# Performance work log

Hardware: AMD Instinct MI355X
Metric: run time of the kernel (lower is better)

## Reference

```python
import jax, jax.numpy as jnp
import numpy as np

M_HIST = 6
LAM = 1e-4
THRESHOLD = 50
BETA = 1.0


def _f_step(z, x, Wh, bh, Wx, bx, Wo, bo):
    # DEQ cell: f(z, x) = tanh(Linear(tanh(h_layer(x) + x_layer(z))))
    # (note: Func.forward(x, z) is called as f(z, x), so h_layer sees the
    #  external input x and x_layer sees the iterate z)
    hidden = jnp.tanh(x @ Wh.T + bh + z @ Wx.T + bx)  # [B,S,H]
    return jnp.tanh(hidden @ Wo.T + bo)               # [B,S,D]


def _anderson(f, x0):
    bsz = x0.shape[0]
    dL = x0.shape[1] * x0.shape[2]
    flat = lambda z: z.reshape(bsz, dL)
    unflat = lambda z: z.reshape(x0.shape)

    X = jnp.zeros((bsz, M_HIST, dL), dtype=x0.dtype)
    F = jnp.zeros((bsz, M_HIST, dL), dtype=x0.dtype)
    F0 = flat(f(x0))
    X = X.at[:, 0].set(flat(x0))
    F = F.at[:, 0].set(F0)
    X = X.at[:, 1].set(F0)
    F = F.at[:, 1].set(flat(f(unflat(F0))))

    lowest = jnp.asarray(1e8, dtype=x0.dtype)
    lowest_x = jnp.zeros((bsz, dL), dtype=x0.dtype)

    for k in range(2, THRESHOLD):  # fixed unrolled solver iterations
        n = min(k, M_HIST)
        G = F[:, :n] - X[:, :n]                       # [B,n,dL]
        GG = jnp.einsum('bnd,bmd->bnm', G, G) + LAM * jnp.eye(n, dtype=x0.dtype)
        H = jnp.zeros((bsz, n + 1, n + 1), dtype=x0.dtype)
        H = H.at[:, 0, 1:].set(1.0)
        H = H.at[:, 1:, 0].set(1.0)
        H = H.at[:, 1:, 1:].set(GG)
        rhs = jnp.zeros((bsz, n + 1, 1), dtype=x0.dtype).at[:, 0, 0].set(1.0)
        alpha = jnp.linalg.solve(H, rhs)[:, 1:, 0]    # [B,n]
        Xk = BETA * jnp.einsum('bn,bnd->bd', alpha, F[:, :n]) \
            + (1.0 - BETA) * jnp.einsum('bn,bnd->bd', alpha, X[:, :n])
        Fk = flat(f(unflat(Xk)))
        X = X.at[:, k % M_HIST].set(Xk)
        F = F.at[:, k % M_HIST].set(Fk)
        abs_diff = jnp.linalg.norm(Fk - Xk)
        rel_diff = abs_diff / (1e-5 + jnp.linalg.norm(Fk))
        better = rel_diff < lowest
        lowest_x = jnp.where(better, Xk, lowest_x)
        lowest = jnp.minimum(rel_diff, lowest)
    return unflat(lowest_x)


def setup_inputs() -> dict:
    key = jax.random.key(0)
    ks = jax.random.split(key, 9)
    B, S, D, H, O = 16384, 31, 14, 50, 1
    sc = lambda fan_in: 1.0 / np.sqrt(fan_in)
    return {
        'x':  jax.random.normal(ks[0], (B, S, D), jnp.float32),
        'Wh': jax.random.normal(ks[1], (H, D), jnp.float32) * sc(D),
        'bh': jax.random.normal(ks[2], (H,), jnp.float32) * sc(D),
        'Wx': jax.random.normal(ks[3], (H, D), jnp.float32) * sc(D),
        'bx': jax.random.normal(ks[4], (H,), jnp.float32) * sc(D),
        'Wo': jax.random.normal(ks[5], (D, H), jnp.float32) * sc(H),
        'bo': jax.random.normal(ks[6], (D,), jnp.float32) * sc(H),
        'Wf': jax.random.normal(ks[7], (O, S * D), jnp.float32) * sc(S * D),
        'bf': jax.random.normal(ks[8], (O,), jnp.float32) * sc(S * D),
    }


def reference(x, Wh, bh, Wx, bx, Wo, bo, Wf, bf):
    f = lambda z: _f_step(z, x, Wh, bh, Wx, bx, Wo, bo)
    z_star = _anderson(f, jnp.zeros_like(x))   # fixed-point solve (no grad)
    z = f(z_star)                              # one extra f application
    out = z.reshape(z.shape[0], -1) @ Wf.T + bf  # [B,1]
    return out
```

## Files before the change

kernel.cpp:

```cpp
#include <hip/hip_runtime.h>
#include <hip/hip_fp16.h>

#define S 31
#define D 14
#define H 50
#define MH 6
#define NB 16384
#define NITER 48
#define LAMR 1e-4f

#define WS_D2   0
#define WS_F2   64
#define WS_WHP  128
#define WS_WXP  928
#define WS_WOT  1728
#define WS_BHX  2528
#define WS_BO   2592
#define WS_OUTK 4096

#ifndef __has_builtin
#define __has_builtin(x) 0
#endif
#if __has_builtin(__builtin_amdgcn_rcpf)
#define FRCP(x) __builtin_amdgcn_rcpf(x)
#else
#define FRCP(x) (1.0f/(x))
#endif

__device__ __forceinline__ float tfast(float x){
  float e = __expf(x + x);
  return 1.f - 2.f * FRCP(e + 1.f);
}

__device__ __forceinline__ float half_red(float v){
  v += __shfl_xor(v, 1, 64);
  v += __shfl_xor(v, 2, 64);
  v += __shfl_xor(v, 4, 64);
  v += __shfl_xor(v, 8, 64);
  v += __shfl_xor(v, 16, 64);
  return v;
}

__global__ void prep_kernel(const float* __restrict__ Wh, const float* __restrict__ bh,
                            const float* __restrict__ Wx, const float* __restrict__ bx,
                            const float* __restrict__ Wo, const float* __restrict__ bo,
                            float* __restrict__ ws){
  int t = threadIdx.x;
  for (int i=t;i<128;i+=256) ws[i]=0.f;
  for (int i=t;i<800;i+=256){
    int h=i>>4, d=i&15;
    ws[WS_WHP+i] = (d<D)? Wh[h*D+d] : 0.f;
    ws[WS_WXP+i] = (d<D)? Wx[h*D+d] : 0.f;
    ws[WS_WOT+i] = (d<D)? Wo[d*H+h] : 0.f;
  }
  for (int i=t;i<64;i+=256) ws[WS_BHX+i] = (i<H)? bh[i]+bx[i] : 0.f;
  for (int i=t;i<16;i+=256) ws[WS_BO+i]  = (i<D)? bo[i] : 0.f;
}

#define FEVAL() do{ \
  float tac[D]; \
  _Pragma("unroll") for (int d_=0; d_<D; ++d_) tac[d_]=bop[d_]; \
  _Pragma("unroll 2") \
  for (int h_=0; h_<H; ++h_){ \
    const float* wxr = wxp + h_*16; \
    const float* wor = wot + h_*16; \
    float a0 = hxr[h_], a1 = 0.f; \
    _Pragma("unroll") for (int d_=0; d_<D; d_+=2){ a0 += xv[d_]*wxr[d_]; a1 += xv[d_+1]*wxr[d_+1]; } \
    float th = tfast(a0+a1); \
    _Pragma("unroll") for (int d_=0; d_<D; ++d_) tac[d_] += th*wor[d_]; \
  } \
  _Pragma("unroll") for (int d_=0; d_<D; ++d_) fv[d_] = tfast(tac[d_]); \
}while(0)

#define UPD(r) do{ \
  _Pragma("unroll") for (int dd_=0;dd_<7;++dd_){ \
    Fh[r][dd_]=__floats2half2_rn(fv[2*dd_],fv[2*dd_+1]); \
    Gh[r][dd_]=__floats2half2_rn(gv[2*dd_],gv[2*dd_+1]); } \
  _Pragma("unroll") for (int j_=0;j_<MH;++j_){ \
    float dl=0.f; \
    _Pragma("unroll") for (int dd_=0;dd_<7;++dd_){ \
      float2 g2=__half22float2(Gh[j_][dd_]); \
      dl += gv[2*dd_]*g2.x + gv[2*dd_+1]*g2.y; } \
    if (!act) dl=0.f; \
    dl = half_red(dl); \
    GG[(r)*6+j_]=dl; GG[j_*6+(r)]=dl; \
  } \
}while(0)

#define ITER(kk, r) do{ \
  float A[36], y[6]; \
  _Pragma("unroll") for (int i_=0;i_<6;++i_){ \
    _Pragma("unroll") for (int j_=0;j_<6;++j_){ \
      float v_ = GG[i_*6+j_]; \
      if (i_==j_) v_ = (i_ < (kk)) ? (v_ + LAMR) : 1e30f; \
      else        v_ = ((i_ < (kk)) && (j_ < (kk))) ? v_ : 0.f; \
      A[i_*6+j_]=v_; } \
    y[i_]=1.f; } \
   \
  _Pragma("unroll") for (int p_=0;p_<6;++p_){ \
    float inv_ = FRCP(A[p_*6+p_]); \
    A[p_*6+p_]=inv_; \
    _Pragma("unroll") for (int i2_=p_+1;i2_<6;++i2_){ \
      float m_ = A[i2_*6+p_]*inv_; \
      _Pragma("unroll") for (int j2_=p_+1;j2_<6;++j2_) A[i2_*6+j2_] -= m_*A[p_*6+j2_]; \
      y[i2_] -= m_*y[p_]; } } \
  _Pragma("unroll") for (int p_=5;p_>=0;--p_){ \
    float ac_=y[p_]; \
    _Pragma("unroll") for (int j2_=p_+1;j2_<6;++j2_) ac_ -= A[p_*6+j2_]*y[j2_]; \
    y[p_]=ac_*A[p_*6+p_]; } \
  float isum = FRCP(y[0]+y[1]+y[2]+y[3]+y[4]+y[5]); \
   \
  _Pragma("unroll") for (int d_=0;d_<D;++d_) xv[d_]=0.f; \
  _Pragma("unroll") for (int j_=0;j_<6;++j_){ \
    float aj_ = y[j_]*isum; \
    _Pragma("unroll") for (int dd_=0;dd_<7;++dd_){ \
      float2 fw_=__half22float2(Fh[j_][dd_]); \
      xv[2*dd_]   += aj_*fw_.x; \
      xv[2*dd_+1] += aj_*fw_.y; } } \
  FEVAL(); \
  float fk2=0.f, d2l=0.f; \
  _Pragma("unroll") for (int d_=0;d_<D;++d_){ gv[d_]=fv[d_]-xv[d_]; fk2 += fv[d_]*fv[d_]; d2l += gv[d_]*gv[d_]; } \
  if (!act){ fk2=0.f; d2l=0.f; } \
  UPD(r); \
  float d2r = half_red(d2l); \
  float f2r = half_red(fk2); \
  float d2w = d2r + __shfl_xor(d2r, 32, 64); \
  float f2w = f2r + __shfl_xor(f2r, 32, 64); \
  if (lane==0){ atomicAdd(&d2p[(kk)-2], d2w); atomicAdd(&f2p[(kk)-2], f2w); } \
  float po=0.f; \
  if (act){ const float* wfr = wf + s*D; \
    _Pragma("unroll") for (int d_=0;d_<D;++d_) po += fv[d_]*wfr[d_]; } \
  po = half_red(po); \
  if (s==0) outk[((kk)-2)*NB + elem] = po; \
}while(0)

__global__ __launch_bounds__(64, 2)
void solver_kernel(const float* __restrict__ x, const float* __restrict__ wf,
                   const float* __restrict__ whp, const float* __restrict__ wxp,
                   const float* __restrict__ wot, const float* __restrict__ bhx,
                   const float* __restrict__ bop,
                   float* __restrict__ outk, float* __restrict__ d2p, float* __restrict__ f2p){
  const int lane = threadIdx.x;
  const int half = lane >> 5;
  const int s    = lane & 31;
  const int elem = blockIdx.x*2 + half;
  const bool act = (s < S);

  __shared__ float hx[2][32][51];

  {
    float xd[D];
#pragma unroll
    for (int d=0; d<D; ++d) xd[d]=0.f;
    if (act){
      const float* xr = x + ((size_t)elem*S + s)*D;
#pragma unroll
      for (int d=0; d<D; ++d) xd[d]=xr[d];
    }
    for (int h=0; h<H; ++h){
      float a0 = bhx[h], a1 = 0.f;
#pragma unroll
      for (int d=0; d<D; d+=2){ a0 += xd[d]*whp[h*16+d]; a1 += xd[d+1]*whp[h*16+d+1]; }
      hx[half][s][h] = a0+a1;
    }
  }
  const float* hxr = &hx[half][s][0];

  __half2 Fh[MH][7], Gh[MH][7];
#pragma unroll
  for (int j=0;j<MH;++j)
#pragma unroll
    for (int dd=0;dd<7;++dd){ Fh[j][dd]=__floats2half2_rn(0.f,0.f); Gh[j][dd]=__floats2half2_rn(0.f,0.f); }
  float GG[36];
#pragma unroll
  for (int i=0;i<36;++i) GG[i]=0.f;

  float xv[D], fv[D], gv[D];

#pragma unroll
  for (int d=0;d<D;++d) xv[d]=0.f;
  FEVAL();
#pragma unroll
  for (int d=0;d<D;++d) gv[d]=fv[d];
  UPD(0);
#pragma unroll
  for (int d=0;d<D;++d) xv[d]=fv[d];
  FEVAL();
#pragma unroll
  for (int d=0;d<D;++d) gv[d]=fv[d]-xv[d];
  UPD(1);

  for (int kb=2; kb<50; kb+=6){
    ITER(kb+0, 2);
    ITER(kb+1, 3);
    ITER(kb+2, 4);
    ITER(kb+3, 5);
    ITER(kb+4, 0);
    ITER(kb+5, 1);
  }
}

__global__ void final_kernel(const float* __restrict__ d2p, const float* __restrict__ f2p,
                             const float* __restrict__ outk, const float* __restrict__ bf,
                             float* __restrict__ out){
  int b = blockIdx.x*blockDim.x + threadIdx.x;
  float best = 1e8f; int kst = 0;
  for (int k=0;k<NITER;++k){
    float rel = sqrtf(d2p[k]) / (1e-5f + sqrtf(f2p[k]));
    if (rel < best){ best = rel; kst = k; }
  }
  out[b] = outk[(size_t)kst*NB + b] + bf[0];
}

extern "C" void kernel_launch(void* const* d_in, const int* in_sizes, int n_in,
                              void* d_out, int out_size, void* d_ws, size_t ws_size,
                              hipStream_t stream){
  const float* x  = (const float*)d_in[0];
  const float* Wh = (const float*)d_in[1];
  const float* bh = (const float*)d_in[2];
  const float* Wx = (const float*)d_in[3];
  const float* bx = (const float*)d_in[4];
  const float* Wo = (const float*)d_in[5];
  const float* bo = (const float*)d_in[6];
  const float* Wf = (const float*)d_in[7];
  const float* bf = (const float*)d_in[8];
  float* ws  = (float*)d_ws;
  float* out = (float*)d_out;

  hipLaunchKernelGGL(prep_kernel, dim3(1), dim3(256), 0, stream, Wh,bh,Wx,bx,Wo,bo,ws);
  hipLaunchKernelGGL(solver_kernel, dim3(NB/2), dim3(64), 0, stream,
                     x, Wf, ws+WS_WHP, ws+WS_WXP, ws+WS_WOT, ws+WS_BHX, ws+WS_BO,
                     ws+WS_OUTK, ws+WS_D2, ws+WS_F2);
  hipLaunchKernelGGL(final_kernel, dim3(NB/256), dim3(256), 0, stream,
                     ws+WS_D2, ws+WS_F2, ws+WS_OUTK, bf, out);
}
```

Baseline: 3.337 ms.

## Rewrite solver in packed fp16 with dot2, sliding history and triangular solve

The DEQ cell now runs in packed half precision using fdot2 instructions with weights pre-packed as half2 (including Wf), instead of scalar fp32 FMAs. The Anderson history becomes a shifted sliding window with a packed upper-triangular Gram matrix, and the 6x6 solve works on the symmetric triangle. The iteration loop is rolled, and blocks grow to 256 threads covering 8 batch elements. These changes aim to cut ALU work and register pressure and to raise occupancy. The cost is extra fp16 rounding in the iterate, hidden state and Gram dot products, which could shift the solver's convergence and accuracy.

```diff
diff --git a/kernel.cpp b/kernel.cpp
--- a/kernel.cpp
+++ b/kernel.cpp
@@ -4,7 +4,6 @@
 #define S 31
 #define D 14
 #define H 50
-#define MH 6
 #define NB 16384
 #define NITER 48
 #define LAMR 1e-4f
@@ -12,141 +11,143 @@
 #define WS_D2   0
 #define WS_F2   64
 #define WS_WHP  128
-#define WS_WXP  928
-#define WS_WOT  1728
-#define WS_BHX  2528
-#define WS_BO   2592
+#define WS_BHX  928
+#define WS_BO   992
+#define WS_WX2  1024
+#define WS_WO2  1424
+#define WS_WF2  1792
 #define WS_OUTK 4096
 
-#ifndef __has_builtin
-#define __has_builtin(x) 0
-#endif
-#if __has_builtin(__builtin_amdgcn_rcpf)
+typedef _Float16 f16x2 __attribute__((ext_vector_type(2)));
+
+#if defined(__has_builtin) && __has_builtin(__builtin_amdgcn_rcpf)
 #define FRCP(x) __builtin_amdgcn_rcpf(x)
 #else
 #define FRCP(x) (1.0f/(x))
 #endif
 
+#define FDOT2(a,b,c) __builtin_amdgcn_fdot2((a),(b),(c),false)
+
+__device__ __forceinline__ f16x2 pkrtz(float a, float b){
+  auto r = __builtin_amdgcn_cvt_pkrtz(a, b);
+  return __builtin_bit_cast(f16x2, r);
+}
+#define PKRTZ(a,b) pkrtz((a),(b))
+
+#define AIJ(i,j) ((i)*6 - ((i)*((i)+1))/2 + (j))
+
 __device__ __forceinline__ float tfast(float x){
   float e = __expf(x + x);
   return 1.f - 2.f * FRCP(e + 1.f);
 }
 
 __device__ __forceinline__ float half_red(float v){
-  v += __shfl_xor(v, 1, 64);
-  v += __shfl_xor(v, 2, 64);
-  v += __shfl_xor(v, 4, 64);
-  v += __shfl_xor(v, 8, 64);
-  v += __shfl_xor(v, 16, 64);
+  v += __shfl_xor(v, 1);
+  v += __shfl_xor(v, 2);
+  v += __shfl_xor(v, 4);
+  v += __shfl_xor(v, 8);
+  v += __shfl_xor(v, 16);
   return v;
 }
 
 __global__ void prep_kernel(const float* __restrict__ Wh, const float* __restrict__ bh,
                             const float* __restrict__ Wx, const float* __restrict__ bx,
                             const float* __restrict__ Wo, const float* __restrict__ bo,
-                            float* __restrict__ ws){
+                            const float* __restrict__ Wf, float* __restrict__ ws){
   int t = threadIdx.x;
   for (int i=t;i<128;i+=256) ws[i]=0.f;
   for (int i=t;i<800;i+=256){
     int h=i>>4, d=i&15;
     ws[WS_WHP+i] = (d<D)? Wh[h*D+d] : 0.f;
-    ws[WS_WXP+i] = (d<D)? Wx[h*D+d] : 0.f;
-    ws[WS_WOT+i] = (d<D)? Wo[d*H+h] : 0.f;
   }
   for (int i=t;i<64;i+=256) ws[WS_BHX+i] = (i<H)? bh[i]+bx[i] : 0.f;
   for (int i=t;i<16;i+=256) ws[WS_BO+i]  = (i<D)? bo[i] : 0.f;
+  __half2* wx2 = (__half2*)(ws + WS_WX2);
+  for (int i=t;i<400;i+=256){
+    int h=i>>3, dd=i&7, d0=2*dd, d1=2*dd+1;
+    float a=(d0<D)?Wx[h*D+d0]:0.f, b=(d1<D)?Wx[h*D+d1]:0.f;
+    wx2[i] = __floats2half2_rn(a,b);
+  }
+  __half2* wo2 = (__half2*)(ws + WS_WO2);
+  for (int i=t;i<364;i+=256){
+    int d=i/26, hh=i-26*d, h0=2*hh, h1=2*hh+1;
+    float a=(hh<25)?Wo[d*H+h0]:0.f, b=(hh<25)?Wo[d*H+h1]:0.f;
+    wo2[i] = __floats2half2_rn(a,b);
+  }
+  __half2* wf2 = (__half2*)(ws + WS_WF2);
+  for (int i=t;i<256;i+=256){
+    int s=i>>3, dd=i&7, d0=2*dd, d1=2*dd+1;
+    float a=(s<S && d0<D)?Wf[s*D+d0]:0.f, b=(s<S && d1<D)?Wf[s*D+d1]:0.f;
+    wf2[i] = __floats2half2_rn(a,b);
+  }
 }
 
 #define FEVAL() do{ \
-  float tac[D]; \
-  _Pragma("unroll") for (int d_=0; d_<D; ++d_) tac[d_]=bop[d_]; \
-  _Pragma("unroll 2") \
-  for (int h_=0; h_<H; ++h_){ \
-    const float* wxr = wxp + h_*16; \
-    const float* wor = wot + h_*16; \
-    float a0 = hxr[h_], a1 = 0.f; \
-    _Pragma("unroll") for (int d_=0; d_<D; d_+=2){ a0 += xv[d_]*wxr[d_]; a1 += xv[d_+1]*wxr[d_+1]; } \
-    float th = tfast(a0+a1); \
-    _Pragma("unroll") for (int d_=0; d_<D; ++d_) tac[d_] += th*wor[d_]; \
+  f16x2 thh[25]; \
+  _Pragma("unroll") \
+  for (int hh_=0; hh_<25; ++hh_){ \
+    float a0_ = hxr[2*hh_], b0_ = hxr[2*hh_+1]; \
+    _Pragma("unroll") for (int q_=0;q_<7;++q_){ \
+      a0_ = FDOT2(xvh[q_], wx2[(2*hh_)*8+q_],   a0_); \
+      b0_ = FDOT2(xvh[q_], wx2[(2*hh_+1)*8+q_], b0_); } \
+    thh[hh_] = PKRTZ(tfast(a0_), tfast(b0_)); \
   } \
-  _Pragma("unroll") for (int d_=0; d_<D; ++d_) fv[d_] = tfast(tac[d_]); \
-}while(0)
-
-#define UPD(r) do{ \
-  _Pragma("unroll") for (int dd_=0;dd_<7;++dd_){ \
-    Fh[r][dd_]=__floats2half2_rn(fv[2*dd_],fv[2*dd_+1]); \
-    Gh[r][dd_]=__floats2half2_rn(gv[2*dd_],gv[2*dd_+1]); } \
-  _Pragma("unroll") for (int j_=0;j_<MH;++j_){ \
-    float dl=0.f; \
-    _Pragma("unroll") for (int dd_=0;dd_<7;++dd_){ \
-      float2 g2=__half22float2(Gh[j_][dd_]); \
-      dl += gv[2*dd_]*g2.x + gv[2*dd_+1]*g2.y; } \
-    if (!act) dl=0.f; \
-    dl = half_red(dl); \
-    GG[(r)*6+j_]=dl; GG[j_*6+(r)]=dl; \
+  _Pragma("unroll") \
+  for (int dp_=0; dp_<7; ++dp_){ \
+    float t0_ = bop[2*dp_], t1_ = bop[2*dp_+1]; \
+    float t0b_ = 0.f, t1b_ = 0.f; \
+    _Pragma("unroll") for (int hh_=0;hh_<25;hh_+=2){ \
+      t0_ = FDOT2(thh[hh_], wo2[(2*dp_)*26+hh_],   t0_); \
+      t1_ = FDOT2(thh[hh_], wo2[(2*dp_+1)*26+hh_], t1_); } \
+    _Pragma("unroll") for (int hh_=1;hh_<25;hh_+=2){ \
+      t0b_ = FDOT2(thh[hh_], wo2[(2*dp_)*26+hh_],   t0b_); \
+      t1b_ = FDOT2(thh[hh_], wo2[(2*dp_+1)*26+hh_], t1b_); } \
+    fvh[dp_] = PKRTZ(tfast(t0_+t0b_), tfast(t1_+t1b_)); \
   } \
 }while(0)
 
-#define ITER(kk, r) do{ \
-  float A[36], y[6]; \
-  _Pragma("unroll") for (int i_=0;i_<6;++i_){ \
-    _Pragma("unroll") for (int j_=0;j_<6;++j_){ \
-      float v_ = GG[i_*6+j_]; \
-      if (i_==j_) v_ = (i_ < (kk)) ? (v_ + LAMR) : 1e30f; \
-      else        v_ = ((i_ < (kk)) && (j_ < (kk))) ? v_ : 0.f; \
-      A[i_*6+j_]=v_; } \
-    y[i_]=1.f; } \
-   \
-  _Pragma("unroll") for (int p_=0;p_<6;++p_){ \
-    float inv_ = FRCP(A[p_*6+p_]); \
-    A[p_*6+p_]=inv_; \
-    _Pragma("unroll") for (int i2_=p_+1;i2_<6;++i2_){ \
-      float m_ = A[i2_*6+p_]*inv_; \
-      _Pragma("unroll") for (int j2_=p_+1;j2_<6;++j2_) A[i2_*6+j2_] -= m_*A[p_*6+j2_]; \
-      y[i2_] -= m_*y[p_]; } } \
-  _Pragma("unroll") for (int p_=5;p_>=0;--p_){ \
-    float ac_=y[p_]; \
-    _Pragma("unroll") for (int j2_=p_+1;j2_<6;++j2_) ac_ -= A[p_*6+j2_]*y[j2_]; \
-    y[p_]=ac_*A[p_*6+p_]; } \
-  float isum = FRCP(y[0]+y[1]+y[2]+y[3]+y[4]+y[5]); \
-   \
-  _Pragma("unroll") for (int d_=0;d_<D;++d_) xv[d_]=0.f; \
-  _Pragma("unroll") for (int j_=0;j_<6;++j_){ \
-    float aj_ = y[j_]*isum; \
-    _Pragma("unroll") for (int dd_=0;dd_<7;++dd_){ \
-      float2 fw_=__half22float2(Fh[j_][dd_]); \
-      xv[2*dd_]   += aj_*fw_.x; \
-      xv[2*dd_+1] += aj_*fw_.y; } } \
-  FEVAL(); \
-  float fk2=0.f, d2l=0.f; \
-  _Pragma("unroll") for (int d_=0;d_<D;++d_){ gv[d_]=fv[d_]-xv[d_]; fk2 += fv[d_]*fv[d_]; d2l += gv[d_]*gv[d_]; } \
-  if (!act){ fk2=0.f; d2l=0.f; } \
-  UPD(r); \
-  float d2r = half_red(d2l); \
-  float f2r = half_red(fk2); \
-  float d2w = d2r + __shfl_xor(d2r, 32, 64); \
-  float f2w = f2r + __shfl_xor(f2r, 32, 64); \
-  if (lane==0){ atomicAdd(&d2p[(kk)-2], d2w); atomicAdd(&f2p[(kk)-2], f2w); } \
-  float po=0.f; \
-  if (act){ const float* wfr = wf + s*D; \
-    _Pragma("unroll") for (int d_=0;d_<D;++d_) po += fv[d_]*wfr[d_]; } \
-  po = half_red(po); \
-  if (s==0) outk[((kk)-2)*NB + elem] = po; \
+#define ZERO_INACT() do{ \
+  if (!act){ \
+    _Pragma("unroll") for (int q_=0;q_<7;++q_){ fvh[q_]=zzv; gvh[q_]=zzv; } \
+  } \
 }while(0)
 
-__global__ __launch_bounds__(64, 2)
-void solver_kernel(const float* __restrict__ x, const float* __restrict__ wf,
-                   const float* __restrict__ whp, const float* __restrict__ wxp,
-                   const float* __restrict__ wot, const float* __restrict__ bhx,
+#define PUSH() do{ \
+  float dnew_[5]; \
+  _Pragma("unroll") for (int j_=0;j_<5;++j_){ \
+    float acc_=0.f; \
+    _Pragma("unroll") for (int q_=0;q_<7;++q_) acc_ = FDOT2(gvh[q_], Gh[(j_+1)*7+q_], acc_); \
+    dnew_[j_] = half_red(acc_); } \
+  d2l=0.f; f2l=0.f; \
+  _Pragma("unroll") for (int q_=0;q_<7;++q_){ \
+    d2l = FDOT2(gvh[q_], gvh[q_], d2l); \
+    f2l = FDOT2(fvh[q_], fvh[q_], f2l); } \
+  d2r = half_red(d2l); f2r = half_red(f2l); \
+  _Pragma("unroll") for (int j_=0;j_<5;++j_) \
+    _Pragma("unroll") for (int q_=0;q_<7;++q_){ \
+      Fh[j_*7+q_] = Fh[(j_+1)*7+q_]; Gh[j_*7+q_] = Gh[(j_+1)*7+q_]; } \
+  _Pragma("unroll") for (int q_=0;q_<7;++q_){ Fh[35+q_]=fvh[q_]; Gh[35+q_]=gvh[q_]; } \
+  _Pragma("unroll") for (int i_=0;i_<5;++i_) \
+    _Pragma("unroll") for (int j_=i_;j_<5;++j_) GG[AIJ(i_,j_)] = GG[AIJ(i_+1,j_+1)]; \
+  _Pragma("unroll") for (int j_=0;j_<5;++j_) GG[AIJ(j_,5)] = dnew_[j_]; \
+  GG[AIJ(5,5)] = d2r; \
+}while(0)
+
+__global__ __launch_bounds__(256, 3)
+void solver_kernel(const float* __restrict__ x,
+                   const float* __restrict__ whp, const float* __restrict__ bhx,
                    const float* __restrict__ bop,
+                   const f16x2* __restrict__ wx2, const f16x2* __restrict__ wo2,
+                   const f16x2* __restrict__ wf2,
                    float* __restrict__ outk, float* __restrict__ d2p, float* __restrict__ f2p){
-  const int lane = threadIdx.x;
-  const int half = lane >> 5;
-  const int s    = lane & 31;
-  const int elem = blockIdx.x*2 + half;
+  const int tid  = threadIdx.x;
+  const int lane = tid & 63;
+  const int s    = tid & 31;
+  const int elem = blockIdx.x*8 + (tid>>5);
   const bool act = (s < S);
 
-  __shared__ float hx[2][32][51];
+  __shared__ float hx_sh[256*51];
+  float* hxw = hx_sh + tid*51;
 
   {
     float xd[D];
@@ -157,46 +158,102 @@
 #pragma unroll
       for (int d=0; d<D; ++d) xd[d]=xr[d];
     }
+#pragma unroll 2
     for (int h=0; h<H; ++h){
       float a0 = bhx[h], a1 = 0.f;
 #pragma unroll
       for (int d=0; d<D; d+=2){ a0 += xd[d]*whp[h*16+d]; a1 += xd[d+1]*whp[h*16+d+1]; }
-      hx[half][s][h] = a0+a1;
-    }
-  }
-  const float* hxr = &hx[half][s][0];
-
-  __half2 Fh[MH][7], Gh[MH][7];
-#pragma unroll
-  for (int j=0;j<MH;++j)
-#pragma unroll
-    for (int dd=0;dd<7;++dd){ Fh[j][dd]=__floats2half2_rn(0.f,0.f); Gh[j][dd]=__floats2half2_rn(0.f,0.f); }
-  float GG[36];
-#pragma unroll
-  for (int i=0;i<36;++i) GG[i]=0.f;
-
-  float xv[D], fv[D], gv[D];
-
-#pragma unroll
-  for (int d=0;d<D;++d) xv[d]=0.f;
+      hxw[h] = a0+a1;
+    }
+  }
+  const float* hxr = hxw;
+  const f16x2 zzv = {(_Float16)0.f, (_Float16)0.f};
+
+  f16x2 Fh[42], Gh[42], xvh[7], fvh[7], gvh[7];
+  float GG[21];
+  float d2l, f2l, d2r, f2r;
+#pragma unroll
+  for (int i=0;i<42;++i){ Fh[i]=zzv; Gh[i]=zzv; }
+#pragma unroll
+  for (int i=0;i<21;++i) GG[i]=0.f;
+
+#pragma unroll
+  for (int q=0;q<7;++q) xvh[q]=zzv;
   FEVAL();
 #pragma unroll
-  for (int d=0;d<D;++d) gv[d]=fv[d];
-  UPD(0);
-#pragma unroll
-  for (int d=0;d<D;++d) xv[d]=fv[d];
+  for (int q=0;q<7;++q) gvh[q]=fvh[q]-xvh[q];
+  ZERO_INACT();
+  PUSH();
+#pragma unroll
+  for (int q=0;q<7;++q) xvh[q]=fvh[q];
   FEVAL();
 #pragma unroll
-  for (int d=0;d<D;++d) gv[d]=fv[d]-xv[d];
-  UPD(1);
-
-  for (int kb=2; kb<50; kb+=6){
-    ITER(kb+0, 2);
-    ITER(kb+1, 3);
-    ITER(kb+2, 4);
-    ITER(kb+3, 5);
-    ITER(kb+4, 0);
-    ITER(kb+5, 1);
+  for (int q=0;q<7;++q) gvh[q]=fvh[q]-xvh[q];
+  ZERO_INACT();
+  PUSH();
+
+#pragma unroll 1
+  for (int kk=2; kk<50; ++kk){
+    float A_[21], invd[6], yv[6];
+    if (kk >= 6){
+#pragma unroll
+      for (int i=0;i<6;++i)
+#pragma unroll
+        for (int j=i;j<6;++j) A_[AIJ(i,j)] = GG[AIJ(i,j)] + ((i==j)?LAMR:0.f);
+    } else {
+      int lo = 6-kk;
+#pragma unroll
+      for (int i=0;i<6;++i)
+#pragma unroll
+        for (int j=i;j<6;++j){
+          float v = GG[AIJ(i,j)] + ((i==j)?LAMR:0.f);
+          A_[AIJ(i,j)] = (i>=lo)? v : ((i==j)?1e30f:0.f);
+        }
+    }
+#pragma unroll
+    for (int i=0;i<6;++i) yv[i]=1.f;
+#pragma unroll
+    for (int p=0;p<6;++p){
+      invd[p] = FRCP(A_[AIJ(p,p)]);
+#pragma unroll
+      for (int i=p+1;i<6;++i){
+        float m = A_[AIJ(p,i)]*invd[p];
+#pragma unroll
+        for (int j=i;j<6;++j) A_[AIJ(i,j)] -= m*A_[AIJ(p,j)];
+        yv[i] -= m*yv[p];
+      }
+    }
+#pragma unroll
+    for (int p=5;p>=0;--p){
+      float acc=yv[p];
+#pragma unroll
+      for (int j=p+1;j<6;++j) acc -= A_[AIJ(p,j)]*yv[j];
+      yv[p]=acc*invd[p];
+    }
+    float isum = FRCP(yv[0]+yv[1]+yv[2]+yv[3]+yv[4]+yv[5]);
+#pragma unroll
+    for (int q=0;q<7;++q) xvh[q]=zzv;
+#pragma unroll
+    for (int j=0;j<6;++j){
+      _Float16 ah = (_Float16)(yv[j]*isum);
+      f16x2 a2 = {ah, ah};
+#pragma unroll
+      for (int q=0;q<7;++q) xvh[q] += a2*Fh[j*7+q];
+    }
+    FEVAL();
+#pragma unroll
+    for (int q=0;q<7;++q) gvh[q]=fvh[q]-xvh[q];
+    ZERO_INACT();
+    PUSH();
+    float po=0.f;
+    const f16x2* wfr = wf2 + s*8;
+#pragma unroll
+    for (int q=0;q<7;++q) po = FDOT2(fvh[q], wfr[q], po);
+    po = half_red(po);
+    float d2w = d2r + __shfl_xor(d2r, 32);
+    float f2w = f2r + __shfl_xor(f2r, 32);
+    if (lane==0){ atomicAdd(&d2p[kk-2], d2w); atomicAdd(&f2p[kk-2], f2w); }
+    if (s==0) outk[(size_t)(kk-2)*NB + elem] = po;
   }
 }
 
@@ -227,9 +284,10 @@
   float* ws  = (float*)d_ws;
   float* out = (float*)d_out;
 
-  hipLaunchKernelGGL(prep_kernel, dim3(1), dim3(256), 0, stream, Wh,bh,Wx,bx,Wo,bo,ws);
-  hipLaunchKernelGGL(solver_kernel, dim3(NB/2), dim3(64), 0, stream,
-                     x, Wf, ws+WS_WHP, ws+WS_WXP, ws+WS_WOT, ws+WS_BHX, ws+WS_BO,
+  hipLaunchKernelGGL(prep_kernel, dim3(1), dim3(256), 0, stream, Wh,bh,Wx,bx,Wo,bo,Wf,ws);
+  hipLaunchKernelGGL(solver_kernel, dim3(NB/8), dim3(256), 0, stream,
+                     x, ws+WS_WHP, ws+WS_BHX, ws+WS_BO,
+                     (const f16x2*)(ws+WS_WX2), (const f16x2*)(ws+WS_WO2), (const f16x2*)(ws+WS_WF2),
                      ws+WS_OUTK, ws+WS_D2, ws+WS_F2);
   hipLaunchKernelGGL(final_kernel, dim3(NB/256), dim3(256), 0, stream,
                      ws+WS_D2, ws+WS_F2, ws+WS_OUTK, bf, out);
```

After: 3.275 ms. About the same (-1.9%).
